# Kernel tuning notes

Hardware: AMD Instinct MI355X
Metric: run time of the kernel (lower is better)

The kernel has to match this reference:

```python
import math
import jax, jax.numpy as jnp
import numpy as np

D_MODEL = 1024
NUM_HEADS = 16
HEAD_DIM = D_MODEL // NUM_HEADS
MAX_REL = 128


def setup_inputs() -> dict:
    key = jax.random.key(0)
    ks = jax.random.split(key, 7)
    B, S = 2, 2048
    s = 1.0 / math.sqrt(D_MODEL)
    return {
        "x": jax.random.normal(ks[0], (B, S, D_MODEL), dtype=jnp.float32),
        "mask": jnp.ones((B, S, S), dtype=jnp.int32),
        "w_q": jax.random.normal(ks[1], (D_MODEL, D_MODEL), dtype=jnp.float32) * s,
        "w_k": jax.random.normal(ks[2], (D_MODEL, D_MODEL), dtype=jnp.float32) * s,
        "w_v": jax.random.normal(ks[3], (D_MODEL, D_MODEL), dtype=jnp.float32) * s,
        "w_o_w": jax.random.normal(ks[4], (D_MODEL, D_MODEL), dtype=jnp.float32) * s,
        "w_o_b": jnp.zeros((D_MODEL,), dtype=jnp.float32),
        "rel_emb": jax.random.normal(ks[5], (2 * MAX_REL + 1, HEAD_DIM), dtype=jnp.float32),
    }


def reference(x, mask, w_q, w_k, w_v, w_o_w, w_o_b, rel_emb):
    B, S, D = x.shape
    H, hd = NUM_HEADS, HEAD_DIM
    scale = math.sqrt(hd)

    def proj(w):  # torch Linear: x @ w.T  -> [B,H,S,hd]
        return (x @ w.T).reshape(B, S, H, hd).transpose(0, 2, 1, 3)

    Q, K, V = proj(w_q), proj(w_k), proj(w_v)

    # content scores (scaled)
    scores = jnp.einsum("bhqd,bhkd->bhqk", Q, K) / scale

    # T5-style relative position bias (NOT scaled, matching source)
    pos = jnp.arange(S)
    dist = jnp.clip(pos[None, :] - pos[:, None], -MAX_REL, MAX_REL) + MAX_REL  # [S,S]
    rel = rel_emb[dist]  # [S,S,hd]
    scores = scores + jnp.einsum("bhqd,qkd->bhqk", Q, rel)

    scores = jnp.where(mask[:, None, :, :] == 0, -1e9, scores)
    attn = jax.nn.softmax(scores, axis=-1)  # [B,H,S,S]

    ctx = jnp.einsum("bhqk,bhkd->bhqd", attn, V)
    ctx = ctx.transpose(0, 2, 1, 3).reshape(B, S, D)
    out = ctx @ w_o_w.T + w_o_b
    return out, attn
```

## Files before the change

kernel.cpp:

```cpp
#include <hip/hip_runtime.h>
#include <hip/hip_bf16.h>

#define B_ 2
#define S_ 2048
#define H_ 16
#define HD_ 64
#define D_ 1024
#define NJ_ 257
#define RSTRIDE_ 264

typedef __bf16 v8bf __attribute__((ext_vector_type(8)));
typedef __bf16 v4bf __attribute__((ext_vector_type(4)));
typedef float  v4f  __attribute__((ext_vector_type(4)));

static __device__ __forceinline__ v4f mfma16(v8bf a, v8bf b, v4f c) {
    return __builtin_amdgcn_mfma_f32_16x16x32_bf16(a, b, c, 0, 0, 0);
}

__global__ void k_prep(const float* __restrict__ x, const float* __restrict__ rel,
                       const float* __restrict__ wq, const float* __restrict__ wk,
                       const float* __restrict__ wv, const float* __restrict__ wo,
                       __bf16* __restrict__ xh, __bf16* __restrict__ xl,
                       __bf16* __restrict__ relh, __bf16* __restrict__ rell,
                       __bf16* __restrict__ wqh, __bf16* __restrict__ wkh,
                       __bf16* __restrict__ wvh, __bf16* __restrict__ woh) {
    const int NX = 1048576;
    const int NR = 4112;
    const int NW = 262144;
    const int total = NX + NR + 4 * NW;
    int i = blockIdx.x * blockDim.x + threadIdx.x;
    const int stride = gridDim.x * blockDim.x;
    for (; i < total; i += stride) {
        if (i < NX + NR) {
            const bool isx = i < NX;
            const int j = isx ? i : i - NX;
            const float* src = isx ? x : rel;
            __bf16* dh = isx ? xh : relh;
            __bf16* dl = isx ? xl : rell;
            const float4 v = ((const float4*)src)[j];
            float vv[4] = {v.x, v.y, v.z, v.w};
            v4bf hv, lv;
#pragma unroll
            for (int e = 0; e < 4; e++) {
                __bf16 hb = (__bf16)vv[e];
                hv[e] = hb;
                lv[e] = (__bf16)(vv[e] - (float)hb);
            }
            *(v4bf*)(dh + 4 * (size_t)j) = hv;
            *(v4bf*)(dl + 4 * (size_t)j) = lv;
        } else {
            const int j = i - NX - NR;
            const int region = j >> 18, idx = j & (NW - 1);
            const float* src = region == 0 ? wq : region == 1 ? wk : region == 2 ? wv : wo;
            __bf16* dst = region == 0 ? wqh : region == 1 ? wkh : region == 2 ? wvh : woh;
            const float4 v = ((const float4*)src)[idx];
            v4bf o = {(__bf16)v.x, (__bf16)v.y, (__bf16)v.z, (__bf16)v.w};
            *(v4bf*)(dst + 4 * (size_t)idx) = o;
        }
    }
}

__global__ void k_rowflag(const int* __restrict__ mask, unsigned char* __restrict__ flags) {
    const int row = blockIdx.x;
    const int4* mp = (const int4*)(mask + (size_t)row * S_);
    int ok = 1;
    for (int i = threadIdx.x; i < S_ / 4; i += blockDim.x) {
        int4 m = mp[i];
        ok &= (m.x != 0) & (m.y != 0) & (m.z != 0) & (m.w != 0);
    }
    int all = __syncthreads_and(ok);
    if (threadIdx.x == 0) flags[row] = (unsigned char)(all != 0);
}

__global__ __launch_bounds__(256) void k_projQKV(const __bf16* __restrict__ xh,
                                                 const __bf16* __restrict__ xl,
                                                 const __bf16* __restrict__ wqh,
                                                 const __bf16* __restrict__ wkh,
                                                 const __bf16* __restrict__ wvh,
                                                 __bf16* __restrict__ Qh,
                                                 __bf16* __restrict__ Ql,
                                                 __bf16* __restrict__ Kh,
                                                 __bf16* __restrict__ Vt) {
    __shared__ __bf16 sXh[64][76], sXl[64][76], sW[64][76];
    const int seg = blockIdx.x >> 4;
    const int n0 = (blockIdx.x & 15) * 64;
    const int m0 = blockIdx.y * 64;
    const __bf16* W = seg == 0 ? wqh : (seg == 1 ? wkh : wvh);
    const int tid = threadIdx.x, lane = tid & 63, wid = tid >> 6;
    const int fr = lane & 15, fo = (lane >> 4) * 8;
    const int srow = tid >> 2, scol = (tid & 3) * 16;
    v4f acc[4] = {};
    for (int k0 = 0; k0 < D_; k0 += 64) {
        const size_t ga = (size_t)(m0 + srow) * D_ + k0 + scol;
        const size_t gb = (size_t)(n0 + srow) * D_ + k0 + scol;
        *(v8bf*)&sXh[srow][scol]     = *(const v8bf*)(xh + ga);
        *(v8bf*)&sXh[srow][scol + 8] = *(const v8bf*)(xh + ga + 8);
        if (seg < 2) {
            *(v8bf*)&sXl[srow][scol]     = *(const v8bf*)(xl + ga);
            *(v8bf*)&sXl[srow][scol + 8] = *(const v8bf*)(xl + ga + 8);
        }
        *(v8bf*)&sW[srow][scol]     = *(const v8bf*)(W + gb);
        *(v8bf*)&sW[srow][scol + 8] = *(const v8bf*)(W + gb + 8);
        __syncthreads();
#pragma unroll
        for (int ks = 0; ks < 2; ks++) {
            v8bf ah = *(const v8bf*)&sXh[wid * 16 + fr][ks * 32 + fo];
            v8bf al;
            if (seg < 2) al = *(const v8bf*)&sXl[wid * 16 + fr][ks * 32 + fo];
#pragma unroll
            for (int nt = 0; nt < 4; nt++) {
                v8bf bb = *(const v8bf*)&sW[nt * 16 + fr][ks * 32 + fo];
                acc[nt] = mfma16(ah, bb, acc[nt]);
                if (seg < 2) acc[nt] = mfma16(al, bb, acc[nt]);
            }
        }
        __syncthreads();
    }
    if (seg == 2) {
#pragma unroll
        for (int nt = 0; nt < 4; nt++)
#pragma unroll
            for (int r = 0; r < 4; r++)
                sXh[wid * 16 + (lane >> 4) * 4 + r][nt * 16 + fr] = (__bf16)acc[nt][r];
        __syncthreads();
        const int c = tid >> 2;
        const int r0 = (tid & 3) * 16;
        v8bf o0, o1;
#pragma unroll
        for (int j = 0; j < 8; j++) {
            o0[j] = sXh[r0 + j][c];
            o1[j] = sXh[r0 + 8 + j][c];
        }
        const int b2 = m0 >> 11;
        const size_t gout = ((size_t)(b2 * D_ + n0 + c)) * S_ + (m0 & 2047) + r0;
        *(v8bf*)(Vt + gout)     = o0;
        *(v8bf*)(Vt + gout + 8) = o1;
    } else {
#pragma unroll
        for (int nt = 0; nt < 4; nt++) {
#pragma unroll
            for (int r = 0; r < 4; r++) {
                const int row = m0 + wid * 16 + (lane >> 4) * 4 + r;
                const int col = n0 + nt * 16 + fr;
                const size_t idx = (size_t)row * D_ + col;
                const float f = acc[nt][r];
                if (seg == 0) {
                    __bf16 hb = (__bf16)f;
                    Qh[idx] = hb;
                    Ql[idx] = (__bf16)(f - (float)hb);
                } else {
                    Kh[idx] = (__bf16)f;
                }
            }
        }
    }
}

__global__ __launch_bounds__(256) void k_relgemm(const __bf16* __restrict__ Qh,
                                                 const __bf16* __restrict__ Ql,
                                                 const __bf16* __restrict__ relh,
                                                 const __bf16* __restrict__ rell,
                                                 float* __restrict__ Rg,
                                                 float* __restrict__ qnorm,
                                                 float* __restrict__ Rmax) {
    const int q0 = blockIdx.x * 64;
    const int bh = blockIdx.y;
    const int b = bh >> 4, h = bh & 15;
    const int tid = threadIdx.x, lane = tid & 63, wid = tid >> 6;
    const int fr = lane & 15, fo = (lane >> 4) * 8;
    const size_t qbase = (size_t)(b * S_ + q0 + wid * 16 + fr) * D_ + h * HD_;
    v8bf qa_h[2], qa_l[2];
#pragma unroll
    for (int ks = 0; ks < 2; ks++) {
        qa_h[ks] = *(const v8bf*)(Qh + qbase + ks * 32 + fo);
        qa_l[ks] = *(const v8bf*)(Ql + qbase + ks * 32 + fo);
    }

    float qs = 0.0f;
#pragma unroll
    for (int ks = 0; ks < 2; ks++)
#pragma unroll
        for (int j = 0; j < 8; j++) {
            const float v = (float)qa_h[ks][j] + (float)qa_l[ks][j];
            qs += v * v;
        }
    qs += __shfl_xor(qs, 16);
    qs += __shfl_xor(qs, 32);
    if ((lane >> 4) == 0) qnorm[(size_t)bh * S_ + q0 + wid * 16 + fr] = sqrtf(qs);

    v4f acc[17] = {};
#pragma unroll
    for (int jt = 0; jt < 17; jt++) {
        int j = jt * 16 + fr;
        if (j > 256) j = 256;
        const size_t rb = (size_t)j * HD_;
#pragma unroll
        for (int ks = 0; ks < 2; ks++) {
            v8bf bh_ = *(const v8bf*)(relh + rb + ks * 32 + fo);
            v8bf bl_ = *(const v8bf*)(rell + rb + ks * 32 + fo);
            acc[jt] = mfma16(qa_h[ks], bh_, acc[jt]);
            acc[jt] = mfma16(qa_h[ks], bl_, acc[jt]);
            acc[jt] = mfma16(qa_l[ks], bh_, acc[jt]);
        }
    }

    float rm[4] = {-3.0e38f, -3.0e38f, -3.0e38f, -3.0e38f};
#pragma unroll
    for (int jt = 0; jt < 17; jt++)
#pragma unroll
        for (int r = 0; r < 4; r++) rm[r] = fmaxf(rm[r], acc[jt][r]);
#pragma unroll
    for (int r = 0; r < 4; r++) {
#pragma unroll
        for (int sh = 1; sh < 16; sh <<= 1) rm[r] = fmaxf(rm[r], __shfl_xor(rm[r], sh));
    }
    if (fr == 0) {
#pragma unroll
        for (int r = 0; r < 4; r++)
            Rmax[(size_t)bh * S_ + q0 + wid * 16 + (lane >> 4) * 4 + r] = rm[r];
    }

    const size_t rowbase = ((size_t)bh * S_ + q0 + wid * 16 + (lane >> 4) * 4) * RSTRIDE_;
#pragma unroll
    for (int jt = 0; jt < 17; jt++) {
        const int j = jt * 16 + fr;
        if (j <= 256) {
#pragma unroll
            for (int r = 0; r < 4; r++)
                Rg[rowbase + (size_t)r * RSTRIDE_ + j] = acc[jt][r];
        }
    }
}

__global__ __launch_bounds__(256) void k_knorm(const __bf16* __restrict__ Kh,
                                               float* __restrict__ Kmax) {
    __shared__ float red[4];
    const int bh = blockIdx.x, b = bh >> 4, h = bh & 15;
    const int tid = threadIdx.x;
    float best = 0.0f;
#pragma unroll
    for (int i = 0; i < 8; i++) {
        const int k = tid + i * 256;
        const __bf16* kr = Kh + (size_t)(b * S_ + k) * D_ + h * HD_;
        float s = 0.0f;
#pragma unroll
        for (int j = 0; j < 8; j++) {
            v8bf v = *(const v8bf*)(kr + j * 8);
#pragma unroll
            for (int e = 0; e < 8; e++) { const float f = (float)v[e]; s += f * f; }
        }
        best = fmaxf(best, s);
    }
#pragma unroll
    for (int sh = 1; sh < 64; sh <<= 1) best = fmaxf(best, __shfl_xor(best, sh));
    if ((tid & 63) == 0) red[tid >> 6] = best;
    __syncthreads();
    if (tid == 0)
        Kmax[bh] = sqrtf(fmaxf(fmaxf(red[0], red[1]), fmaxf(red[2], red[3])));
}

__global__ __launch_bounds__(512, 4) void k_attnE(const __bf16* __restrict__ Qh,
                                                  const __bf16* __restrict__ Ql,
                                                  const __bf16* __restrict__ Kh,
                                                  const __bf16* __restrict__ Vt,
                                                  const float* __restrict__ Rg,
                                                  const int* __restrict__ mask,
                                                  const unsigned char* __restrict__ flags,
                                                  const float* __restrict__ qnorm,
                                                  const float* __restrict__ Rmax,
                                                  const float* __restrict__ Kmax,
                                                  __bf16* __restrict__ E,
                                                  float* __restrict__ attn,
                                                  __bf16* __restrict__ ctx) {
    __shared__ __bf16 sK[2][64][76], sV[2][64][76], sP[128][76];
    __shared__ float sLi[128];
    const int flat = blockIdx.x;
    const int swz = (flat & 7) * 64 + (flat >> 3);
    const int qt = swz & 15, bh = swz >> 4;
    const int b = bh >> 4, h = bh & 15;
    const int q0 = qt * 128;
    const int tid = threadIdx.x, lane = tid & 63, w = tid >> 6;
    const int fr = lane & 15, fq = lane >> 4, fo = fq * 8;
    const int myrow = w * 16 + fq * 4;
    const int srow = tid >> 3, sc8 = (tid & 7) * 8;

    const size_t qbase = (size_t)(b * S_ + q0 + w * 16 + fr) * D_ + h * HD_;
    v8bf qa_h[2], qa_l[2];
#pragma unroll
    for (int ks = 0; ks < 2; ks++) {
        qa_h[ks] = *(const v8bf*)(Qh + qbase + ks * 32 + fo);
        qa_l[ks] = *(const v8bf*)(Ql + qbase + ks * 32 + fo);
    }

    const int qg0 = q0 + myrow;
    const size_t rbase0 = ((size_t)bh * S_ + qg0) * RSTRIDE_;
    const size_t mbase0 = ((size_t)b * S_ + qg0) * S_;
    float rcL[4], rcR[4], mhat[4];
    int flr[4];
    const float km = Kmax[bh] * 0.125f;
#pragma unroll
    for (int r = 0; r < 4; r++) {
        rcL[r] = Rg[rbase0 + (size_t)r * RSTRIDE_];
        rcR[r] = Rg[rbase0 + (size_t)r * RSTRIDE_ + 256];
        flr[r] = flags[(size_t)b * S_ + qg0 + r];
        mhat[r] = Rmax[(size_t)bh * S_ + qg0 + r] +
                  qnorm[(size_t)bh * S_ + qg0 + r] * km + 0.5f;
    }

    const int erow = w * 16 + (lane >> 2);
    const int ecol = (lane & 3) * 16;
    __bf16* ebase = E + ((size_t)bh * S_ + q0 + erow) * S_ + ecol;

    const __bf16* kgbase = Kh + (size_t)(b * S_ + srow) * D_ + h * HD_ + sc8;
    const __bf16* vgbase = Vt + (size_t)(b * D_ + h * HD_ + srow) * S_ + sc8;
    v8bf rk = *(const v8bf*)(kgbase);
    v8bf rv = *(const v8bf*)(vgbase);
    *(v8bf*)&sK[0][srow][sc8] = rk;
    *(v8bf*)&sV[0][srow][sc8] = rv;
    rk = *(const v8bf*)(kgbase + (size_t)64 * D_);
    rv = *(const v8bf*)(vgbase + 64);
    __syncthreads();

    float lrun[4] = {0.0f, 0.0f, 0.0f, 0.0f};
    v4f acc2[4] = {};
    int cur = 0;
    for (int kc = 0; kc < 32; kc++) {
        const int k0 = kc * 64;
        v4f acc[4] = {};
#pragma unroll
        for (int ct = 0; ct < 4; ct++) {
#pragma unroll
            for (int ks = 0; ks < 2; ks++) {
                v8bf kb = *(const v8bf*)&sK[cur][ct * 16 + fr][ks * 32 + fo];
                acc[ct] = mfma16(qa_h[ks], kb, acc[ct]);
                acc[ct] = mfma16(qa_l[ks], kb, acc[ct]);
            }
        }
        const bool band = (kc >= 2 * qt - 3) && (kc <= 2 * qt + 3);
        const bool left = kc < 2 * qt;
#pragma unroll
        for (int r = 0; r < 4; r++) {
            const int qg = qg0 + r;
#pragma unroll
            for (int ct = 0; ct < 4; ct++) {
                const int k = k0 + ct * 16 + fr;
                float bias;
                if (band) {
                    const int dd = k - qg;
                    const int j = dd < -128 ? 0 : (dd > 128 ? 256 : dd + 128);
                    bias = Rg[rbase0 + (size_t)r * RSTRIDE_ + j];
                } else {
                    bias = left ? rcL[r] : rcR[r];
                }
                float sv = acc[ct][r] * 0.125f + bias;
                if (!flr[r] && mask[mbase0 + (size_t)r * S_ + k] == 0) sv = -1e9f;
                const float e = __expf(sv - mhat[r]);
                lrun[r] += e;
                sP[myrow + r][ct * 16 + fr] = (__bf16)e;
            }
        }
#pragma unroll
        for (int ks = 0; ks < 2; ks++) {
            v8bf pa = *(const v8bf*)&sP[w * 16 + fr][ks * 32 + fo];
#pragma unroll
            for (int ct = 0; ct < 4; ct++) {
                v8bf vb = *(const v8bf*)&sV[cur][ct * 16 + fr][ks * 32 + fo];
                acc2[ct] = mfma16(pa, vb, acc2[ct]);
            }
        }
        *(v8bf*)(ebase + k0)     = *(const v8bf*)&sP[erow][ecol];
        *(v8bf*)(ebase + k0 + 8) = *(const v8bf*)&sP[erow][ecol + 8];
        if (kc < 31) {
            *(v8bf*)&sK[cur ^ 1][srow][sc8] = rk;
            *(v8bf*)&sV[cur ^ 1][srow][sc8] = rv;
        }
        if (kc < 30) {
            rk = *(const v8bf*)(kgbase + (size_t)(k0 + 128) * D_);
            rv = *(const v8bf*)(vgbase + k0 + 128);
        }
        __builtin_amdgcn_sched_barrier(0);
        asm volatile("s_waitcnt lgkmcnt(0)" ::: "memory");
        __builtin_amdgcn_s_barrier();
        __builtin_amdgcn_sched_barrier(0);
        cur ^= 1;
    }

    float invl[4];
#pragma unroll
    for (int r = 0; r < 4; r++) {
#pragma unroll
        for (int sh = 1; sh < 16; sh <<= 1) lrun[r] += __shfl_xor(lrun[r], sh);
        invl[r] = 1.0f / (lrun[r] + 1e-37f);
    }
    if (fr == 0) {
#pragma unroll
        for (int r = 0; r < 4; r++) sLi[myrow + r] = invl[r];
    }

#pragma unroll
    for (int ct = 0; ct < 4; ct++) {
#pragma unroll
        for (int r = 0; r < 4; r++) {
            const int qg = qg0 + r;
            const int d = ct * 16 + fr;
            ctx[(size_t)(b * S_ + qg) * D_ + h * HD_ + d] = (__bf16)(acc2[ct][r] * invl[r]);
        }
    }

    asm volatile("s_waitcnt vmcnt(0)" ::: "memory");
    __syncthreads();

    const __bf16* Eblk = E + ((size_t)bh * S_ + q0) * S_;
    float* ablk = attn + ((size_t)bh * S_ + q0) * S_;
#pragma unroll 4
    for (int it = 0; it < 64; it++) {
        const int g = tid + it * 512;
        const int row = g >> 8;
        const int col8 = (g & 255) * 8;
        const float inv = sLi[row];
        const v8bf e = *(const v8bf*)(Eblk + (size_t)row * S_ + col8);
        float4 o0, o1;
        o0.x = (float)e[0] * inv; o0.y = (float)e[1] * inv;
        o0.z = (float)e[2] * inv; o0.w = (float)e[3] * inv;
        o1.x = (float)e[4] * inv; o1.y = (float)e[5] * inv;
        o1.z = (float)e[6] * inv; o1.w = (float)e[7] * inv;
        *(float4*)(ablk + (size_t)row * S_ + col8)     = o0;
        *(float4*)(ablk + (size_t)row * S_ + col8 + 4) = o1;
    }
}

__global__ __launch_bounds__(256) void k_outproj(const __bf16* __restrict__ A,
                                                 const __bf16* __restrict__ Bw,
                                                 const float* __restrict__ bias,
                                                 float* __restrict__ out) {
    __shared__ __bf16 sA[64][76], sB[64][76];
    const int n0 = blockIdx.x * 64;
    const int m0 = blockIdx.y * 64;
    const int tid = threadIdx.x, lane = tid & 63, wid = tid >> 6;
    const int fr = lane & 15, fo = (lane >> 4) * 8;
    const int srow = tid >> 2, scol = (tid & 3) * 16;
    v4f acc[4] = {};
    for (int k0 = 0; k0 < D_; k0 += 64) {
        const size_t ga = (size_t)(m0 + srow) * D_ + k0 + scol;
        const size_t gb = (size_t)(n0 + srow) * D_ + k0 + scol;
        *(v8bf*)&sA[srow][scol]     = *(const v8bf*)(A + ga);
        *(v8bf*)&sA[srow][scol + 8] = *(const v8bf*)(A + ga + 8);
        *(v8bf*)&sB[srow][scol]     = *(const v8bf*)(Bw + gb);
        *(v8bf*)&sB[srow][scol + 8] = *(const v8bf*)(Bw + gb + 8);
        __syncthreads();
#pragma unroll
        for (int ks = 0; ks < 2; ks++) {
            v8bf a = *(const v8bf*)&sA[wid * 16 + fr][ks * 32 + fo];
#pragma unroll
            for (int nt = 0; nt < 4; nt++) {
                v8bf bb = *(const v8bf*)&sB[nt * 16 + fr][ks * 32 + fo];
                acc[nt] = mfma16(a, bb, acc[nt]);
            }
        }
        __syncthreads();
    }
#pragma unroll
    for (int nt = 0; nt < 4; nt++) {
        const float bv = bias[n0 + nt * 16 + fr];
#pragma unroll
        for (int r = 0; r < 4; r++) {
            const int row = m0 + wid * 16 + (lane >> 4) * 4 + r;
            out[(size_t)row * D_ + n0 + nt * 16 + fr] = acc[nt][r] + bv;
        }
    }
}

extern "C" void kernel_launch(void* const* d_in, const int* in_sizes, int n_in,
                              void* d_out, int out_size, void* d_ws, size_t ws_size,
                              hipStream_t stream) {
    (void)in_sizes; (void)n_in; (void)out_size; (void)ws_size;
    const float* x    = (const float*)d_in[0];
    const int*   mask = (const int*)d_in[1];
    const float* wq   = (const float*)d_in[2];
    const float* wk   = (const float*)d_in[3];
    const float* wv   = (const float*)d_in[4];
    const float* wo   = (const float*)d_in[5];
    const float* wob  = (const float*)d_in[6];
    const float* rel  = (const float*)d_in[7];
    float* out  = (float*)d_out;
    float* attn = out + (size_t)B_ * S_ * D_;

    char* p = (char*)d_ws;
    auto alloc = [&](size_t bytes) -> char* {
        char* r = p;
        p += (bytes + 255) & ~(size_t)255;
        return r;
    };
    const size_t BSD = (size_t)B_ * S_ * D_;
    const size_t DD  = (size_t)D_ * D_;
    const size_t BHS = (size_t)B_ * H_ * S_;
    __bf16* xh   = (__bf16*)alloc(BSD * 2);
    __bf16* xl   = (__bf16*)alloc(BSD * 2);
    __bf16* wqh  = (__bf16*)alloc(DD * 2);
    __bf16* wkh  = (__bf16*)alloc(DD * 2);
    __bf16* wvh  = (__bf16*)alloc(DD * 2);
    __bf16* woh  = (__bf16*)alloc(DD * 2);
    __bf16* relh = (__bf16*)alloc((size_t)NJ_ * HD_ * 2);
    __bf16* rell = (__bf16*)alloc((size_t)NJ_ * HD_ * 2);
    __bf16* Qh   = (__bf16*)alloc(BSD * 2);
    __bf16* Ql   = (__bf16*)alloc(BSD * 2);
    __bf16* Kh   = (__bf16*)alloc(BSD * 2);
    __bf16* Vt   = (__bf16*)alloc(BSD * 2);
    float*  Rg   = (float*)alloc(BHS * RSTRIDE_ * 4);
    float*  qn   = (float*)alloc(BHS * 4);
    float*  Rmax = (float*)alloc(BHS * 4);
    float*  Kmax = (float*)alloc((size_t)B_ * H_ * 4);
    __bf16* E    = (__bf16*)alloc((size_t)B_ * H_ * S_ * S_ * 2);
    __bf16* ctx  = (__bf16*)alloc(BSD * 2);
    unsigned char* flags = (unsigned char*)alloc((size_t)B_ * S_);

    k_prep<<<2048, 256, 0, stream>>>(x, rel, wq, wk, wv, wo,
                                     xh, xl, relh, rell, wqh, wkh, wvh, woh);

    k_rowflag<<<B_ * S_, 256, 0, stream>>>(mask, flags);

    k_projQKV<<<dim3(48, B_ * S_ / 64), 256, 0, stream>>>(xh, xl, wqh, wkh, wvh,
                                                          Qh, Ql, Kh, Vt);

    k_relgemm<<<dim3(S_ / 64, B_ * H_), 256, 0, stream>>>(Qh, Ql, relh, rell, Rg, qn, Rmax);

    k_knorm<<<B_ * H_, 256, 0, stream>>>(Kh, Kmax);

    k_attnE<<<512, 512, 0, stream>>>(Qh, Ql, Kh, Vt, Rg, mask, flags, qn, Rmax, Kmax,
                                     E, attn, ctx);

    k_outproj<<<dim3(D_ / 64, B_ * S_ / 64), 256, 0, stream>>>(ctx, woh, wob, out);
}
```

Measured before the change: 551.5 us.

## Software-pipeline QK^T MFMA with previous chunk's softmax and PV in attention kernel

Restructures the attention main loop so that the QK^T MFMAs for chunk kc are issued while the exp/bias/mask work and PV MFMAs for chunk kc-1 run, keeping the previous scores in a second accumulator set. V shared buffers grow to triple-buffering so the V tile for the lagged chunk is not overwritten, and the last chunk is handled in an epilogue. The goal is to overlap matrix-core work with the VALU-heavy softmax section. It costs more registers and more LDS, which may reduce occupancy under the 512-thread, 4-block launch bound.

```diff
diff --git a/kernel.cpp b/kernel.cpp
--- a/kernel.cpp
+++ b/kernel.cpp
@@ -272,7 +272,7 @@
                                                   __bf16* __restrict__ E,
                                                   float* __restrict__ attn,
                                                   __bf16* __restrict__ ctx) {
-    __shared__ __bf16 sK[2][64][76], sV[2][64][76], sP[128][76];
+    __shared__ __bf16 sK[2][64][76], sV[3][64][76], sP[128][76];
     __shared__ float sLi[128];
     const int flat = blockIdx.x;
     const int swz = (flat & 7) * 64 + (flat >> 3);
@@ -323,27 +323,85 @@
 
     float lrun[4] = {0.0f, 0.0f, 0.0f, 0.0f};
     v4f acc2[4] = {};
-    int cur = 0;
+    v4f accO[4] = {};
+
     for (int kc = 0; kc < 32; kc++) {
         const int k0 = kc * 64;
-        v4f acc[4] = {};
+        v4f accN[4] = {};
 #pragma unroll
         for (int ct = 0; ct < 4; ct++) {
 #pragma unroll
             for (int ks = 0; ks < 2; ks++) {
-                v8bf kb = *(const v8bf*)&sK[cur][ct * 16 + fr][ks * 32 + fo];
-                acc[ct] = mfma16(qa_h[ks], kb, acc[ct]);
-                acc[ct] = mfma16(qa_l[ks], kb, acc[ct]);
-            }
-        }
-        const bool band = (kc >= 2 * qt - 3) && (kc <= 2 * qt + 3);
-        const bool left = kc < 2 * qt;
+                v8bf kb = *(const v8bf*)&sK[kc & 1][ct * 16 + fr][ks * 32 + fo];
+                accN[ct] = mfma16(qa_h[ks], kb, accN[ct]);
+                accN[ct] = mfma16(qa_l[ks], kb, accN[ct]);
+            }
+        }
+        if (kc > 0) {
+            const int kcd = kc - 1;
+            const int k0d = kcd * 64;
+            const bool band = (kcd >= 2 * qt - 3) && (kcd <= 2 * qt + 3);
+            const bool left = kcd < 2 * qt;
+#pragma unroll
+            for (int r = 0; r < 4; r++) {
+                const int qg = qg0 + r;
+#pragma unroll
+                for (int ct = 0; ct < 4; ct++) {
+                    const int k = k0d + ct * 16 + fr;
+                    float bias;
+                    if (band) {
+                        const int dd = k - qg;
+                        const int j = dd < -128 ? 0 : (dd > 128 ? 256 : dd + 128);
+                        bias = Rg[rbase0 + (size_t)r * RSTRIDE_ + j];
+                    } else {
+                        bias = left ? rcL[r] : rcR[r];
+                    }
+                    float sv = accO[ct][r] * 0.125f + bias;
+                    if (!flr[r] && mask[mbase0 + (size_t)r * S_ + k] == 0) sv = -1e9f;
+                    const float e = __expf(sv - mhat[r]);
+                    lrun[r] += e;
+                    sP[myrow + r][ct * 16 + fr] = (__bf16)e;
+                }
+            }
+#pragma unroll
+            for (int ks = 0; ks < 2; ks++) {
+                v8bf pa = *(const v8bf*)&sP[w * 16 + fr][ks * 32 + fo];
+#pragma unroll
+                for (int ct = 0; ct < 4; ct++) {
+                    v8bf vb = *(const v8bf*)&sV[kcd % 3][ct * 16 + fr][ks * 32 + fo];
+                    acc2[ct] = mfma16(pa, vb, acc2[ct]);
+                }
+            }
+            *(v8bf*)(ebase + k0d)     = *(const v8bf*)&sP[erow][ecol];
+            *(v8bf*)(ebase + k0d + 8) = *(const v8bf*)&sP[erow][ecol + 8];
+        }
+        if (kc < 31) {
+            *(v8bf*)&sK[(kc + 1) & 1][srow][sc8] = rk;
+            *(v8bf*)&sV[(kc + 1) % 3][srow][sc8] = rv;
+        }
+        if (kc < 30) {
+            rk = *(const v8bf*)(kgbase + (size_t)(k0 + 128) * D_);
+            rv = *(const v8bf*)(vgbase + k0 + 128);
+        }
+        __builtin_amdgcn_sched_barrier(0);
+        asm volatile("s_waitcnt lgkmcnt(0)" ::: "memory");
+        __builtin_amdgcn_s_barrier();
+        __builtin_amdgcn_sched_barrier(0);
+#pragma unroll
+        for (int ct = 0; ct < 4; ct++) accO[ct] = accN[ct];
+    }
+
+    {
+        const int kcd = 31;
+        const int k0d = kcd * 64;
+        const bool band = (kcd >= 2 * qt - 3) && (kcd <= 2 * qt + 3);
+        const bool left = kcd < 2 * qt;
 #pragma unroll
         for (int r = 0; r < 4; r++) {
             const int qg = qg0 + r;
 #pragma unroll
             for (int ct = 0; ct < 4; ct++) {
-                const int k = k0 + ct * 16 + fr;
+                const int k = k0d + ct * 16 + fr;
                 float bias;
                 if (band) {
                     const int dd = k - qg;
@@ -352,7 +410,7 @@
                 } else {
                     bias = left ? rcL[r] : rcR[r];
                 }
-                float sv = acc[ct][r] * 0.125f + bias;
+                float sv = accO[ct][r] * 0.125f + bias;
                 if (!flr[r] && mask[mbase0 + (size_t)r * S_ + k] == 0) sv = -1e9f;
                 const float e = __expf(sv - mhat[r]);
                 lrun[r] += e;
@@ -364,25 +422,12 @@
             v8bf pa = *(const v8bf*)&sP[w * 16 + fr][ks * 32 + fo];
 #pragma unroll
             for (int ct = 0; ct < 4; ct++) {
-                v8bf vb = *(const v8bf*)&sV[cur][ct * 16 + fr][ks * 32 + fo];
+                v8bf vb = *(const v8bf*)&sV[kcd % 3][ct * 16 + fr][ks * 32 + fo];
                 acc2[ct] = mfma16(pa, vb, acc2[ct]);
             }
         }
-        *(v8bf*)(ebase + k0)     = *(const v8bf*)&sP[erow][ecol];
-        *(v8bf*)(ebase + k0 + 8) = *(const v8bf*)&sP[erow][ecol + 8];
-        if (kc < 31) {
-            *(v8bf*)&sK[cur ^ 1][srow][sc8] = rk;
-            *(v8bf*)&sV[cur ^ 1][srow][sc8] = rv;
-        }
-        if (kc < 30) {
-            rk = *(const v8bf*)(kgbase + (size_t)(k0 + 128) * D_);
-            rv = *(const v8bf*)(vgbase + k0 + 128);
-        }
-        __builtin_amdgcn_sched_barrier(0);
-        asm volatile("s_waitcnt lgkmcnt(0)" ::: "memory");
-        __builtin_amdgcn_s_barrier();
-        __builtin_amdgcn_sched_barrier(0);
-        cur ^= 1;
+        *(v8bf*)(ebase + k0d)     = *(const v8bf*)&sP[erow][ecol];
+        *(v8bf*)(ebase + k0d + 8) = *(const v8bf*)&sP[erow][ecol + 8];
     }
 
     float invl[4];
```

New measurement: 558.4 us. No clear change (+1.2%).

## Split attention columns across twice as many waves per block

Applied to the files above, without the earlier changes.

Raises the attention block from 512 to 1024 threads, with each wave pair sharing a 16-row strip and each wave handling half of the 64 key/value columns. K and V tile loads are split between the two halves of the block, and the row sums are combined through shared memory. A second barrier is added before the PV step so the next tile's shared-memory stores can be issued earlier. The goal is more waves in flight to hide the exp, mask and E-store latency, in exchange for an extra barrier per iteration and launch bounds of (1024,4) that may not be achievable given register pressure.

```diff
diff --git a/kernel.cpp b/kernel.cpp
--- a/kernel.cpp
+++ b/kernel.cpp
@@ -259,20 +259,21 @@
         Kmax[bh] = sqrtf(fmaxf(fmaxf(red[0], red[1]), fmaxf(red[2], red[3])));
 }
 
-__global__ __launch_bounds__(512, 4) void k_attnE(const __bf16* __restrict__ Qh,
-                                                  const __bf16* __restrict__ Ql,
-                                                  const __bf16* __restrict__ Kh,
-                                                  const __bf16* __restrict__ Vt,
-                                                  const float* __restrict__ Rg,
-                                                  const int* __restrict__ mask,
-                                                  const unsigned char* __restrict__ flags,
-                                                  const float* __restrict__ qnorm,
-                                                  const float* __restrict__ Rmax,
-                                                  const float* __restrict__ Kmax,
-                                                  __bf16* __restrict__ E,
-                                                  float* __restrict__ attn,
-                                                  __bf16* __restrict__ ctx) {
+__global__ __launch_bounds__(1024, 4) void k_attnE(const __bf16* __restrict__ Qh,
+                                                   const __bf16* __restrict__ Ql,
+                                                   const __bf16* __restrict__ Kh,
+                                                   const __bf16* __restrict__ Vt,
+                                                   const float* __restrict__ Rg,
+                                                   const int* __restrict__ mask,
+                                                   const unsigned char* __restrict__ flags,
+                                                   const float* __restrict__ qnorm,
+                                                   const float* __restrict__ Rmax,
+                                                   const float* __restrict__ Kmax,
+                                                   __bf16* __restrict__ E,
+                                                   float* __restrict__ attn,
+                                                   __bf16* __restrict__ ctx) {
     __shared__ __bf16 sK[2][64][76], sV[2][64][76], sP[128][76];
+    __shared__ float sLsum[2][128];
     __shared__ float sLi[128];
     const int flat = blockIdx.x;
     const int swz = (flat & 7) * 64 + (flat >> 3);
@@ -280,11 +281,11 @@
     const int b = bh >> 4, h = bh & 15;
     const int q0 = qt * 128;
     const int tid = threadIdx.x, lane = tid & 63, w = tid >> 6;
-    const int fr = lane & 15, fq = lane >> 4, fo = fq * 8;
-    const int myrow = w * 16 + fq * 4;
-    const int srow = tid >> 3, sc8 = (tid & 7) * 8;
-
-    const size_t qbase = (size_t)(b * S_ + q0 + w * 16 + fr) * D_ + h * HD_;
+    const int wr = w >> 1, wc = w & 1;
+    const int fr = lane & 15, fq = (lane >> 4) & 3, fo = fq * 8;
+    const int myrow = wr * 16 + fq * 4;
+
+    const size_t qbase = (size_t)(b * S_ + q0 + wr * 16 + fr) * D_ + h * HD_;
     v8bf qa_h[2], qa_l[2];
 #pragma unroll
     for (int ks = 0; ks < 2; ks++) {
@@ -307,31 +308,40 @@
                   qnorm[(size_t)bh * S_ + qg0 + r] * km + 0.5f;
     }
 
-    const int erow = w * 16 + (lane >> 2);
-    const int ecol = (lane & 3) * 16;
-    __bf16* ebase = E + ((size_t)bh * S_ + q0 + erow) * S_ + ecol;
-
-    const __bf16* kgbase = Kh + (size_t)(b * S_ + srow) * D_ + h * HD_ + sc8;
-    const __bf16* vgbase = Vt + (size_t)(b * D_ + h * HD_ + srow) * S_ + sc8;
-    v8bf rk = *(const v8bf*)(kgbase);
-    v8bf rv = *(const v8bf*)(vgbase);
-    *(v8bf*)&sK[0][srow][sc8] = rk;
-    *(v8bf*)&sV[0][srow][sc8] = rv;
-    rk = *(const v8bf*)(kgbase + (size_t)64 * D_);
-    rv = *(const v8bf*)(vgbase + 64);
+    const int erow = w * 8 + (lane >> 3);
+    const int ec = (lane & 7) * 8;
+    __bf16* ebase = E + ((size_t)bh * S_ + q0 + erow) * S_ + ec;
+
+    const int st = (w < 8) ? tid : tid - 512;
+    const int srow = st >> 3, sc8 = (st & 7) * 8;
+    const __bf16* gptr;
+    size_t gstep;
+    if (w < 8) {
+        gptr = Kh + (size_t)(b * S_ + srow) * D_ + h * HD_ + sc8;
+        gstep = (size_t)64 * D_;
+    } else {
+        gptr = Vt + (size_t)(b * D_ + h * HD_ + srow) * S_ + sc8;
+        gstep = 64;
+    }
+    {
+        v8bf r0 = *(const v8bf*)(gptr);
+        if (w < 8) *(v8bf*)&sK[0][srow][sc8] = r0;
+        else       *(v8bf*)&sV[0][srow][sc8] = r0;
+    }
+    v8bf rg = *(const v8bf*)(gptr + gstep);
     __syncthreads();
 
     float lrun[4] = {0.0f, 0.0f, 0.0f, 0.0f};
-    v4f acc2[4] = {};
+    v4f acc2[2] = {};
     int cur = 0;
     for (int kc = 0; kc < 32; kc++) {
         const int k0 = kc * 64;
-        v4f acc[4] = {};
-#pragma unroll
-        for (int ct = 0; ct < 4; ct++) {
+        v4f acc[2] = {};
+#pragma unroll
+        for (int ct = 0; ct < 2; ct++) {
 #pragma unroll
             for (int ks = 0; ks < 2; ks++) {
-                v8bf kb = *(const v8bf*)&sK[cur][ct * 16 + fr][ks * 32 + fo];
+                v8bf kb = *(const v8bf*)&sK[cur][wc * 32 + ct * 16 + fr][ks * 32 + fo];
                 acc[ct] = mfma16(qa_h[ks], kb, acc[ct]);
                 acc[ct] = mfma16(qa_l[ks], kb, acc[ct]);
             }
@@ -342,8 +352,8 @@
         for (int r = 0; r < 4; r++) {
             const int qg = qg0 + r;
 #pragma unroll
-            for (int ct = 0; ct < 4; ct++) {
-                const int k = k0 + ct * 16 + fr;
+            for (int ct = 0; ct < 2; ct++) {
+                const int k = k0 + wc * 32 + ct * 16 + fr;
                 float bias;
                 if (band) {
                     const int dd = k - qg;
@@ -356,28 +366,28 @@
                 if (!flr[r] && mask[mbase0 + (size_t)r * S_ + k] == 0) sv = -1e9f;
                 const float e = __expf(sv - mhat[r]);
                 lrun[r] += e;
-                sP[myrow + r][ct * 16 + fr] = (__bf16)e;
-            }
-        }
+                sP[myrow + r][wc * 32 + ct * 16 + fr] = (__bf16)e;
+            }
+        }
+        if (kc < 31) {
+            if (w < 8) *(v8bf*)&sK[cur ^ 1][srow][sc8] = rg;
+            else       *(v8bf*)&sV[cur ^ 1][srow][sc8] = rg;
+        }
+        if (kc < 30) rg = *(const v8bf*)(gptr + (size_t)(kc + 2) * gstep);
+        __builtin_amdgcn_sched_barrier(0);
+        asm volatile("s_waitcnt lgkmcnt(0)" ::: "memory");
+        __builtin_amdgcn_s_barrier();
+        __builtin_amdgcn_sched_barrier(0);
 #pragma unroll
         for (int ks = 0; ks < 2; ks++) {
-            v8bf pa = *(const v8bf*)&sP[w * 16 + fr][ks * 32 + fo];
-#pragma unroll
-            for (int ct = 0; ct < 4; ct++) {
-                v8bf vb = *(const v8bf*)&sV[cur][ct * 16 + fr][ks * 32 + fo];
+            v8bf pa = *(const v8bf*)&sP[wr * 16 + fr][ks * 32 + fo];
+#pragma unroll
+            for (int ct = 0; ct < 2; ct++) {
+                v8bf vb = *(const v8bf*)&sV[cur][wc * 32 + ct * 16 + fr][ks * 32 + fo];
                 acc2[ct] = mfma16(pa, vb, acc2[ct]);
             }
         }
-        *(v8bf*)(ebase + k0)     = *(const v8bf*)&sP[erow][ecol];
-        *(v8bf*)(ebase + k0 + 8) = *(const v8bf*)&sP[erow][ecol + 8];
-        if (kc < 31) {
-            *(v8bf*)&sK[cur ^ 1][srow][sc8] = rk;
-            *(v8bf*)&sV[cur ^ 1][srow][sc8] = rv;
-        }
-        if (kc < 30) {
-            rk = *(const v8bf*)(kgbase + (size_t)(k0 + 128) * D_);
-            rv = *(const v8bf*)(vgbase + k0 + 128);
-        }
+        *(v8bf*)(ebase + k0) = *(const v8bf*)&sP[erow][ec];
         __builtin_amdgcn_sched_barrier(0);
         asm volatile("s_waitcnt lgkmcnt(0)" ::: "memory");
         __builtin_amdgcn_s_barrier();
@@ -385,24 +395,31 @@
         cur ^= 1;
     }
 
+#pragma unroll
+    for (int r = 0; r < 4; r++) {
+#pragma unroll
+        for (int sh = 1; sh < 16; sh <<= 1) lrun[r] += __shfl_xor(lrun[r], sh);
+    }
+    if (fr == 0) {
+#pragma unroll
+        for (int r = 0; r < 4; r++) sLsum[wc][myrow + r] = lrun[r];
+    }
+    __syncthreads();
     float invl[4];
 #pragma unroll
-    for (int r = 0; r < 4; r++) {
-#pragma unroll
-        for (int sh = 1; sh < 16; sh <<= 1) lrun[r] += __shfl_xor(lrun[r], sh);
-        invl[r] = 1.0f / (lrun[r] + 1e-37f);
-    }
-    if (fr == 0) {
+    for (int r = 0; r < 4; r++)
+        invl[r] = 1.0f / (sLsum[0][myrow + r] + sLsum[1][myrow + r] + 1e-37f);
+    if (wc == 0 && fr == 0) {
 #pragma unroll
         for (int r = 0; r < 4; r++) sLi[myrow + r] = invl[r];
     }
 
 #pragma unroll
-    for (int ct = 0; ct < 4; ct++) {
+    for (int ct = 0; ct < 2; ct++) {
 #pragma unroll
         for (int r = 0; r < 4; r++) {
             const int qg = qg0 + r;
-            const int d = ct * 16 + fr;
+            const int d = wc * 32 + ct * 16 + fr;
             ctx[(size_t)(b * S_ + qg) * D_ + h * HD_ + d] = (__bf16)(acc2[ct][r] * invl[r]);
         }
     }
@@ -413,8 +430,8 @@
     const __bf16* Eblk = E + ((size_t)bh * S_ + q0) * S_;
     float* ablk = attn + ((size_t)bh * S_ + q0) * S_;
 #pragma unroll 4
-    for (int it = 0; it < 64; it++) {
-        const int g = tid + it * 512;
+    for (int it = 0; it < 32; it++) {
+        const int g = tid + it * 1024;
         const int row = g >> 8;
         const int col8 = (g & 255) * 8;
         const float inv = sLi[row];
@@ -526,8 +543,8 @@
 
     k_knorm<<<B_ * H_, 256, 0, stream>>>(Kh, Kmax);
 
-    k_attnE<<<512, 512, 0, stream>>>(Qh, Ql, Kh, Vt, Rg, mask, flags, qn, Rmax, Kmax,
-                                     E, attn, ctx);
+    k_attnE<<<512, 1024, 0, stream>>>(Qh, Ql, Kh, Vt, Rg, mask, flags, qn, Rmax, Kmax,
+                                      E, attn, ctx);
 
     k_outproj<<<dim3(D_ / 64, B_ * S_ / 64), 256, 0, stream>>>(ctx, woh, wob, out);
 }
```

Result: no change. 562.4 us (+2.0%).
